# Kernel optimization log

Measured on AMD Instinct MI355X. Metric: run time of the kernel, lower is better.

The kernel has to match this reference:

```python
import jax, jax.numpy as jnp
import numpy as np

OUT_FEATURES = 11008
IN_FEATURES = 4096
GROUP_SIZE = 32
N_GROUPS = OUT_FEATURES * IN_FEATURES // GROUP_SIZE  # 1409024
LEVELS = jnp.array([-1.0, -0.333, 0.333, 1.0], dtype=jnp.float32)


def setup_inputs() -> dict:
    key = jax.random.key(0)
    k1, k2, k3, k4 = jax.random.split(key, 4)
    x = jax.random.normal(k1, (16, IN_FEATURES), dtype=jnp.float32)
    weight_q2 = jax.random.randint(k2, (N_GROUPS, GROUP_SIZE // 4), 0, 256, dtype=jnp.int32)
    weight_norm = jax.random.uniform(k3, (N_GROUPS, 1), dtype=jnp.float32).astype(jnp.float16)
    bias = jax.random.normal(k4, (OUT_FEATURES,), dtype=jnp.float32)
    return {"x": x, "weight_q2": weight_q2, "weight_norm": weight_norm, "bias": bias}


def _dequantize_2bit(packed, norm):
    # packed: [G, group/4] int; element at group-column 4*k+i comes from bits [2i:2i+2) of packed[:, k]
    shifts = jnp.array([0, 2, 4, 6], dtype=jnp.int32)
    codes = (packed[:, :, None] >> shifts[None, None, :]) & 3  # [G, group/4, 4]
    x_q = LEVELS[codes].reshape(packed.shape[0], -1)  # [G, group]
    return x_q * norm.astype(jnp.float32)  # per-group scale


def reference(x, weight_q2, weight_norm, bias):
    weight = _dequantize_2bit(weight_q2, weight_norm).reshape(OUT_FEATURES, IN_FEATURES).astype(x.dtype)
    return x @ weight.T + bias.astype(x.dtype)
```

## Files before the change

### kernel.cpp

```cpp
#include <hip/hip_runtime.h>
#include <hip/hip_fp16.h>

#define OUTF 11008
#define INF  4096
#define NTILES 688

typedef unsigned int uint;
typedef __attribute__((ext_vector_type(8))) _Float16 f16x8;
typedef __attribute__((ext_vector_type(4))) float f32x4;

typedef __attribute__((address_space(1))) void gvoid_t;
typedef __attribute__((address_space(3))) void svoid_t;

union UA { uint4 u4; uint u[4]; f16x8 v; };
union UH { uint u; __half2 h; };
union USH { unsigned short s; __half h; };

#define WAITV(n) asm volatile("s_waitcnt vmcnt(" #n ")" ::: "memory")
#define WAITL()  asm volatile("s_waitcnt lgkmcnt(0)" ::: "memory")
#define SBAR()   __builtin_amdgcn_sched_barrier(0)
#define FENCE()  asm volatile("" ::: "memory")
#define BARRIER() { FENCE(); __builtin_amdgcn_s_barrier(); FENCE(); }

__global__ __launch_bounds__(256, 4) void lin2bit_kernel(
    const float* __restrict__ x, const int* __restrict__ wq,
    const float* __restrict__ wn, const float* __restrict__ bias,
    float* __restrict__ out)
{
  __shared__ __align__(16) char lds[34816];
  char* LUT = lds;
  char* NL  = lds + 2048;
  char* X0  = lds + 10240;
  char* X1  = lds + 18432;
  char* W0  = lds + 26624;
  char* W1  = lds + 30720;

  const int tid = threadIdx.x;
  const int wv  = tid >> 6;
  const int l   = tid & 63;
  const int col = l & 15;
  const int q   = l >> 4;
  const int o0  = (int)blockIdx.x << 4;

  const char* xb  = (const char*)x;
  const char* wqb = (const char*)wq;
  const char* wnb = (const char*)wn;

  {
#pragma unroll
    for (int ii = 0; ii < 2; ++ii) {
      const int i = wv * 2 + ii;
      const int r = 2 * i + (l >> 5);
      const char* src = wnb + (size_t)(o0 + r) * 512 + (((l & 31) ^ (r & 7)) << 4);
      __builtin_amdgcn_global_load_lds((gvoid_t*)src,
                                       (svoid_t*)(NL + i * 1024 + l * 16), 16, 0, 0);
    }
  }
  FENCE();

#define XLOAD(c, xr) { \
    _Pragma("unroll") \
    for (int rr = 0; rr < 4; ++rr) { \
      const int r = wv * 4 + rr; \
      const float* srcp = (const float*)(xb + (size_t)r * 16384 + (size_t)(c) * 1024) + l * 4; \
      asm volatile("global_load_dwordx4 %0, %1, off" \
                   : "=&v"((xr)[rr]) : "v"(srcp) : "memory"); \
    } }

#define XWRITE(buf, xr) { \
    _Pragma("unroll") \
    for (int rr = 0; rr < 4; ++rr) { \
      const int r = wv * 4 + rr; \
      UH h0, h1; \
      h0.h = __floats2half2_rn((xr)[rr].x, (xr)[rr].y); \
      h1.h = __floats2half2_rn((xr)[rr].z, (xr)[rr].w); \
      *(uint2*)((buf) + r * 512 + (((l >> 1) ^ (r & 7)) << 4) + (l & 1) * 8) = \
          make_uint2(h0.u, h1.u); \
    } }

#define WSTAGE(c, buf) { \
    const int r = wv * 4 + (l >> 4); \
    const char* src = wqb + (size_t)(o0 + r) * 4096 + (size_t)(c) * 256 \
                      + (((l & 15) ^ (r & 7)) << 4); \
    __builtin_amdgcn_global_load_lds((gvoid_t*)src, \
                                     (svoid_t*)((buf) + wv * 1024 + l * 16), 16, 0, 0); }

  float4 xrA[4], xrB[4];
  XLOAD(0, xrA);   FENCE();
  WSTAGE(0, W0);   FENCE();
  XLOAD(1, xrB);   FENCE();
  WSTAGE(1, W1);   FENCE();

  {
    USH h0, h1, h2, h3;
    h0.h = __float2half(-1.0f);  h1.h = __float2half(-0.333f);
    h2.h = __float2half(0.333f); h3.h = __float2half(1.0f);
    const uint hv[4] = {h0.s, h1.s, h2.s, h3.s};
#pragma unroll
    for (int e = 0; e < 4; ++e) {
      const int idx = e * 64 + l;
      const uint lo = hv[idx & 3]        | (hv[(idx >> 2) & 3] << 16);
      const uint hi = hv[(idx >> 4) & 3] | (hv[(idx >> 6) & 3] << 16);
      *(uint2*)(LUT + idx * 8) = make_uint2(lo, hi);
    }
  }

  WAITV(5); SBAR();
  XWRITE(X0, xrA);
  WAITL(); BARRIER();

  f32x4 acc = {0.f, 0.f, 0.f, 0.f};
  const int c7 = col & 7;

#define COMPUTE(c, xs, ws) { \
    const float2 nn = *(const float2*)(NL + col * 512 \
                        + ((((c) * 2 + (wv >> 1)) ^ c7) << 4) + (wv & 1) * 8); \
    _Pragma("unroll") \
    for (int jj = 0; jj < 2; ++jj) { \
      const int g = wv * 2 + jj; \
      const float nv = jj ? nn.y : nn.x; \
      UH nvh; nvh.h = __floats2half2_rn(nv, nv); \
      const uint2 p = *(const uint2*)((ws) + col * 256 \
                        + (((g * 2 + (q >> 1)) ^ c7) << 4) + (q & 1) * 8); \
      UA A; A.u4 = *(const uint4*)((xs) + col * 512 + (((g * 4 + q) ^ c7) << 4)); \
      const uint2 e0 = *(const uint2*)(LUT + ((size_t)(uint)p.x << 3)); \
      const uint2 e1 = *(const uint2*)(LUT + ((size_t)(uint)p.y << 3)); \
      UH a0, a1, a2, a3, b0, b1, b2, b3; \
      a0.u = e0.x; a1.u = e0.y; a2.u = e1.x; a3.u = e1.y; \
      b0.h = __hmul2(a0.h, nvh.h); b1.h = __hmul2(a1.h, nvh.h); \
      b2.h = __hmul2(a2.h, nvh.h); b3.h = __hmul2(a3.h, nvh.h); \
      UA B; B.u[0] = b0.u; B.u[1] = b1.u; B.u[2] = b2.u; B.u[3] = b3.u; \
      acc = __builtin_amdgcn_mfma_f32_16x16x32_f16(A.v, B.v, acc, 0, 0, 0); \
    } }

#define ITER_FULL(c, XC, WC, XN, XRC, XRN) \
  COMPUTE(c, XC, WC) \
  XLOAD((c) + 2, XRC);  FENCE(); \
  BARRIER(); \
  WSTAGE((c) + 2, WC);  FENCE(); \
  WAITV(5); SBAR(); \
  XWRITE(XN, XRN); \
  WAITL(); BARRIER();

  ITER_FULL(0,  X0, W0, X1, xrA, xrB)
  ITER_FULL(1,  X1, W1, X0, xrB, xrA)
  ITER_FULL(2,  X0, W0, X1, xrA, xrB)
  ITER_FULL(3,  X1, W1, X0, xrB, xrA)
  ITER_FULL(4,  X0, W0, X1, xrA, xrB)
  ITER_FULL(5,  X1, W1, X0, xrB, xrA)
  ITER_FULL(6,  X0, W0, X1, xrA, xrB)
  ITER_FULL(7,  X1, W1, X0, xrB, xrA)
  ITER_FULL(8,  X0, W0, X1, xrA, xrB)
  ITER_FULL(9,  X1, W1, X0, xrB, xrA)
  ITER_FULL(10, X0, W0, X1, xrA, xrB)
  ITER_FULL(11, X1, W1, X0, xrB, xrA)
  ITER_FULL(12, X0, W0, X1, xrA, xrB)
  ITER_FULL(13, X1, W1, X0, xrB, xrA)
  COMPUTE(14, X0, W0)
  BARRIER();
  WAITV(0); SBAR();
  XWRITE(X1, xrB);
  WAITL(); BARRIER();
  COMPUTE(15, X1, W1)
#undef ITER_FULL
#undef COMPUTE
#undef XLOAD
#undef XWRITE
#undef WSTAGE

  __syncthreads();
  float* red = (float*)lds;
  red[wv * 256 +   0 + l] = acc[0];
  red[wv * 256 +  64 + l] = acc[1];
  red[wv * 256 + 128 + l] = acc[2];
  red[wv * 256 + 192 + l] = acc[3];
  __syncthreads();
  const int t = tid;
  const float s = red[t] + red[256 + t] + red[512 + t] + red[768 + t];
  const int m  = ((t & 63) >> 4) * 4 + (t >> 6);
  const int oc = t & 15;
  out[(size_t)m * OUTF + o0 + oc] = s + bias[o0 + oc];
}

extern "C" void kernel_launch(void* const* d_in, const int* in_sizes, int n_in,
                              void* d_out, int out_size, void* d_ws, size_t ws_size,
                              hipStream_t stream) {
  (void)in_sizes; (void)n_in; (void)out_size; (void)d_ws; (void)ws_size;
  const float* x    = (const float*)d_in[0];
  const int*   wq   = (const int*)d_in[1];
  const float* wn   = (const float*)d_in[2];
  const float* bias = (const float*)d_in[3];
  float*       out  = (float*)d_out;
  lin2bit_kernel<<<dim3(NTILES), dim3(256), 0, stream>>>(x, wq, wn, bias, out);
}
```

Baseline: 19.66 us.

## Process two 16-row output tiles per block to reuse staged activations

Each block now computes 32 output features instead of 16, so the grid is halved and every activation chunk converted to fp16 in LDS feeds two weight tiles and two accumulators. This is meant to cut the redundant per-block x loads and conversions, and the per-block setup. In exchange, LDS grows to about 50KB, the occupancy hint drops from 4 to 3 blocks, and only 344 blocks are launched, which could leave compute units underfilled.

```diff
diff --git a/kernel.cpp b/kernel.cpp
--- a/kernel.cpp
+++ b/kernel.cpp
@@ -3,7 +3,7 @@
 
 #define OUTF 11008
 #define INF  4096
-#define NTILES 688
+#define NBLK 344
 
 typedef unsigned int uint;
 typedef __attribute__((ext_vector_type(8))) _Float16 f16x8;
@@ -22,41 +22,43 @@
 #define FENCE()  asm volatile("" ::: "memory")
 #define BARRIER() { FENCE(); __builtin_amdgcn_s_barrier(); FENCE(); }
 
-__global__ __launch_bounds__(256, 4) void lin2bit_kernel(
+__global__ __launch_bounds__(256, 3) void lin2bit_kernel(
     const float* __restrict__ x, const int* __restrict__ wq,
     const float* __restrict__ wn, const float* __restrict__ bias,
     float* __restrict__ out)
 {
-  __shared__ __align__(16) char lds[34816];
+  __shared__ __align__(16) char lds[51200];
   char* LUT = lds;
-  char* NL  = lds + 2048;
-  char* X0  = lds + 10240;
-  char* X1  = lds + 18432;
-  char* W0  = lds + 26624;
-  char* W1  = lds + 30720;
+  char* NLa = lds + 2048;
+  char* NLb = lds + 10240;
+  char* X0  = lds + 18432;
+  char* X1  = lds + 26624;
+  char* W0a = lds + 34816;
+  char* W0b = lds + 38912;
+  char* W1a = lds + 43008;
+  char* W1b = lds + 47104;
 
   const int tid = threadIdx.x;
   const int wv  = tid >> 6;
   const int l   = tid & 63;
   const int col = l & 15;
   const int q   = l >> 4;
-  const int o0  = (int)blockIdx.x << 4;
+  const int o0a = (int)blockIdx.x << 5;
+  const int o0b = o0a + 16;
 
   const char* xb  = (const char*)x;
   const char* wqb = (const char*)wq;
   const char* wnb = (const char*)wn;
 
-  {
-#pragma unroll
-    for (int ii = 0; ii < 2; ++ii) {
-      const int i = wv * 2 + ii;
-      const int r = 2 * i + (l >> 5);
-      const char* src = wnb + (size_t)(o0 + r) * 512 + (((l & 31) ^ (r & 7)) << 4);
-      __builtin_amdgcn_global_load_lds((gvoid_t*)src,
-                                       (svoid_t*)(NL + i * 1024 + l * 16), 16, 0, 0);
-    }
-  }
-  FENCE();
+#define NSTAGE(o0t, nl) { \
+    _Pragma("unroll") \
+    for (int ii = 0; ii < 2; ++ii) { \
+      const int i = wv * 2 + ii; \
+      const int r = 2 * i + (l >> 5); \
+      const char* src = wnb + (size_t)((o0t) + r) * 512 + (((l & 31) ^ (r & 7)) << 4); \
+      __builtin_amdgcn_global_load_lds((gvoid_t*)src, \
+                                       (svoid_t*)((nl) + i * 1024 + l * 16), 16, 0, 0); \
+    } }
 
 #define XLOAD(c, xr) { \
     _Pragma("unroll") \
@@ -78,18 +80,19 @@
           make_uint2(h0.u, h1.u); \
     } }
 
-#define WSTAGE(c, buf) { \
+#define WSTAGE(c, buf, o0t) { \
     const int r = wv * 4 + (l >> 4); \
-    const char* src = wqb + (size_t)(o0 + r) * 4096 + (size_t)(c) * 256 \
+    const char* src = wqb + (size_t)((o0t) + r) * 4096 + (size_t)(c) * 256 \
                       + (((l & 15) ^ (r & 7)) << 4); \
     __builtin_amdgcn_global_load_lds((gvoid_t*)src, \
                                      (svoid_t*)((buf) + wv * 1024 + l * 16), 16, 0, 0); }
 
   float4 xrA[4], xrB[4];
-  XLOAD(0, xrA);   FENCE();
-  WSTAGE(0, W0);   FENCE();
-  XLOAD(1, xrB);   FENCE();
-  WSTAGE(1, W1);   FENCE();
+  NSTAGE(o0a, NLa);  NSTAGE(o0b, NLb);  FENCE();
+  XLOAD(0, xrA);     FENCE();
+  WSTAGE(0, W0a, o0a); WSTAGE(0, W0b, o0b); FENCE();
+  XLOAD(1, xrB);     FENCE();
+  WSTAGE(1, W1a, o0a); WSTAGE(1, W1b, o0b); FENCE();
 
   {
     USH h0, h1, h2, h3;
@@ -105,15 +108,16 @@
     }
   }
 
-  WAITV(5); SBAR();
+  WAITV(6); SBAR();
   XWRITE(X0, xrA);
   WAITL(); BARRIER();
 
-  f32x4 acc = {0.f, 0.f, 0.f, 0.f};
+  f32x4 accA = {0.f, 0.f, 0.f, 0.f};
+  f32x4 accB = {0.f, 0.f, 0.f, 0.f};
   const int c7 = col & 7;
 
-#define COMPUTE(c, xs, ws) { \
-    const float2 nn = *(const float2*)(NL + col * 512 \
+#define COMPUTE(c, xs, ws, nl, accv) { \
+    const float2 nn = *(const float2*)((nl) + col * 512 \
                         + ((((c) * 2 + (wv >> 1)) ^ c7) << 4) + (wv & 1) * 8); \
     _Pragma("unroll") \
     for (int jj = 0; jj < 2; ++jj) { \
@@ -130,56 +134,75 @@
       b0.h = __hmul2(a0.h, nvh.h); b1.h = __hmul2(a1.h, nvh.h); \
       b2.h = __hmul2(a2.h, nvh.h); b3.h = __hmul2(a3.h, nvh.h); \
       UA B; B.u[0] = b0.u; B.u[1] = b1.u; B.u[2] = b2.u; B.u[3] = b3.u; \
-      acc = __builtin_amdgcn_mfma_f32_16x16x32_f16(A.v, B.v, acc, 0, 0, 0); \
-    } }
-
-#define ITER_FULL(c, XC, WC, XN, XRC, XRN) \
-  COMPUTE(c, XC, WC) \
+      (accv) = __builtin_amdgcn_mfma_f32_16x16x32_f16(A.v, B.v, (accv), 0, 0, 0); \
+    } }
+
+#define ITER_FULL(c, XC, WCa, WCb, XN, XRC, XRN) \
+  COMPUTE(c, XC, WCa, NLa, accA) \
+  COMPUTE(c, XC, WCb, NLb, accB) \
   XLOAD((c) + 2, XRC);  FENCE(); \
   BARRIER(); \
-  WSTAGE((c) + 2, WC);  FENCE(); \
-  WAITV(5); SBAR(); \
+  WSTAGE((c) + 2, WCa, o0a); WSTAGE((c) + 2, WCb, o0b); FENCE(); \
+  WAITV(6); SBAR(); \
   XWRITE(XN, XRN); \
   WAITL(); BARRIER();
 
-  ITER_FULL(0,  X0, W0, X1, xrA, xrB)
-  ITER_FULL(1,  X1, W1, X0, xrB, xrA)
-  ITER_FULL(2,  X0, W0, X1, xrA, xrB)
-  ITER_FULL(3,  X1, W1, X0, xrB, xrA)
-  ITER_FULL(4,  X0, W0, X1, xrA, xrB)
-  ITER_FULL(5,  X1, W1, X0, xrB, xrA)
-  ITER_FULL(6,  X0, W0, X1, xrA, xrB)
-  ITER_FULL(7,  X1, W1, X0, xrB, xrA)
-  ITER_FULL(8,  X0, W0, X1, xrA, xrB)
-  ITER_FULL(9,  X1, W1, X0, xrB, xrA)
-  ITER_FULL(10, X0, W0, X1, xrA, xrB)
-  ITER_FULL(11, X1, W1, X0, xrB, xrA)
-  ITER_FULL(12, X0, W0, X1, xrA, xrB)
-  ITER_FULL(13, X1, W1, X0, xrB, xrA)
-  COMPUTE(14, X0, W0)
+  ITER_FULL(0,  X0, W0a, W0b, X1, xrA, xrB)
+  ITER_FULL(1,  X1, W1a, W1b, X0, xrB, xrA)
+  ITER_FULL(2,  X0, W0a, W0b, X1, xrA, xrB)
+  ITER_FULL(3,  X1, W1a, W1b, X0, xrB, xrA)
+  ITER_FULL(4,  X0, W0a, W0b, X1, xrA, xrB)
+  ITER_FULL(5,  X1, W1a, W1b, X0, xrB, xrA)
+  ITER_FULL(6,  X0, W0a, W0b, X1, xrA, xrB)
+  ITER_FULL(7,  X1, W1a, W1b, X0, xrB, xrA)
+  ITER_FULL(8,  X0, W0a, W0b, X1, xrA, xrB)
+  ITER_FULL(9,  X1, W1a, W1b, X0, xrB, xrA)
+  ITER_FULL(10, X0, W0a, W0b, X1, xrA, xrB)
+  ITER_FULL(11, X1, W1a, W1b, X0, xrB, xrA)
+  ITER_FULL(12, X0, W0a, W0b, X1, xrA, xrB)
+  ITER_FULL(13, X1, W1a, W1b, X0, xrB, xrA)
+  COMPUTE(14, X0, W0a, NLa, accA)
+  COMPUTE(14, X0, W0b, NLb, accB)
   BARRIER();
   WAITV(0); SBAR();
   XWRITE(X1, xrB);
   WAITL(); BARRIER();
-  COMPUTE(15, X1, W1)
+  COMPUTE(15, X1, W1a, NLa, accA)
+  COMPUTE(15, X1, W1b, NLb, accB)
 #undef ITER_FULL
 #undef COMPUTE
 #undef XLOAD
 #undef XWRITE
 #undef WSTAGE
-
-  __syncthreads();
+#undef NSTAGE
+
   float* red = (float*)lds;
-  red[wv * 256 +   0 + l] = acc[0];
-  red[wv * 256 +  64 + l] = acc[1];
-  red[wv * 256 + 128 + l] = acc[2];
-  red[wv * 256 + 192 + l] = acc[3];
-  __syncthreads();
-  const int t = tid;
-  const float s = red[t] + red[256 + t] + red[512 + t] + red[768 + t];
-  const int m  = ((t & 63) >> 4) * 4 + (t >> 6);
-  const int oc = t & 15;
-  out[(size_t)m * OUTF + o0 + oc] = s + bias[o0 + oc];
+  __syncthreads();
+  red[wv * 256 +   0 + l] = accA[0];
+  red[wv * 256 +  64 + l] = accA[1];
+  red[wv * 256 + 128 + l] = accA[2];
+  red[wv * 256 + 192 + l] = accA[3];
+  __syncthreads();
+  {
+    const int t = tid;
+    const float s = red[t] + red[256 + t] + red[512 + t] + red[768 + t];
+    const int m  = ((t & 63) >> 4) * 4 + (t >> 6);
+    const int oc = t & 15;
+    out[(size_t)m * OUTF + o0a + oc] = s + bias[o0a + oc];
+  }
+  __syncthreads();
+  red[wv * 256 +   0 + l] = accB[0];
+  red[wv * 256 +  64 + l] = accB[1];
+  red[wv * 256 + 128 + l] = accB[2];
+  red[wv * 256 + 192 + l] = accB[3];
+  __syncthreads();
+  {
+    const int t = tid;
+    const float s = red[t] + red[256 + t] + red[512 + t] + red[768 + t];
+    const int m  = ((t & 63) >> 4) * 4 + (t >> 6);
+    const int oc = t & 15;
+    out[(size_t)m * OUTF + o0b + oc] = s + bias[o0b + oc];
+  }
 }
 
 extern "C" void kernel_launch(void* const* d_in, const int* in_sizes, int n_in,
@@ -191,5 +214,5 @@
   const float* wn   = (const float*)d_in[2];
   const float* bias = (const float*)d_in[3];
   float*       out  = (float*)d_out;
-  lin2bit_kernel<<<dim3(NTILES), dim3(256), 0, stream>>>(x, wq, wn, bias, out);
+  lin2bit_kernel<<<dim3(NBLK), dim3(256), 0, stream>>>(x, wq, wn, bias, out);
 }
```

Result: slower. 20.23 us (+2.9%).

## Replace LDS dequant LUT with per-group register shift table and preload norms

Applied to the files above, without the earlier changes.

Drops the 256-entry LDS lookup table and its hmul2 scaling. Each group now builds a 64-bit register table of the four pre-scaled fp16 levels and extracts every weight with a 64-bit shift followed by a pack. The per-group norms are loaded straight into registers at kernel start instead of being staged through LDS, which shrinks LDS use and removes two LDS reads per group. The cost is more VALU shift and pack work per element and 32 extra VGPRs to hold the norms. Rounding also changes slightly, since the product is now rounded once from fp32 instead of twice in fp16.

```diff
diff --git a/kernel.cpp b/kernel.cpp
--- a/kernel.cpp
+++ b/kernel.cpp
@@ -6,6 +6,7 @@
 #define NTILES 688
 
 typedef unsigned int uint;
+typedef unsigned long long ull;
 typedef __attribute__((ext_vector_type(8))) _Float16 f16x8;
 typedef __attribute__((ext_vector_type(4))) float f32x4;
 
@@ -14,7 +15,6 @@
 
 union UA { uint4 u4; uint u[4]; f16x8 v; };
 union UH { uint u; __half2 h; };
-union USH { unsigned short s; __half h; };
 
 #define WAITV(n) asm volatile("s_waitcnt vmcnt(" #n ")" ::: "memory")
 #define WAITL()  asm volatile("s_waitcnt lgkmcnt(0)" ::: "memory")
@@ -27,13 +27,11 @@
     const float* __restrict__ wn, const float* __restrict__ bias,
     float* __restrict__ out)
 {
-  __shared__ __align__(16) char lds[34816];
-  char* LUT = lds;
-  char* NL  = lds + 2048;
-  char* X0  = lds + 10240;
-  char* X1  = lds + 18432;
-  char* W0  = lds + 26624;
-  char* W1  = lds + 30720;
+  __shared__ __align__(16) char lds[24576];
+  char* X0 = lds;
+  char* X1 = lds + 8192;
+  char* W0 = lds + 16384;
+  char* W1 = lds + 20480;
 
   const int tid = threadIdx.x;
   const int wv  = tid >> 6;
@@ -44,19 +42,6 @@
 
   const char* xb  = (const char*)x;
   const char* wqb = (const char*)wq;
-  const char* wnb = (const char*)wn;
-
-  {
-#pragma unroll
-    for (int ii = 0; ii < 2; ++ii) {
-      const int i = wv * 2 + ii;
-      const int r = 2 * i + (l >> 5);
-      const char* src = wnb + (size_t)(o0 + r) * 512 + (((l & 31) ^ (r & 7)) << 4);
-      __builtin_amdgcn_global_load_lds((gvoid_t*)src,
-                                       (svoid_t*)(NL + i * 1024 + l * 16), 16, 0, 0);
-    }
-  }
-  FENCE();
 
 #define XLOAD(c, xr) { \
     _Pragma("unroll") \
@@ -85,25 +70,23 @@
     __builtin_amdgcn_global_load_lds((gvoid_t*)src, \
                                      (svoid_t*)((buf) + wv * 1024 + l * 16), 16, 0, 0); }
 
+  float2 nf2[16];
+  {
+    const float* np = wn + (size_t)(o0 + col) * 128 + 2 * wv;
+#pragma unroll
+    for (int c = 0; c < 16; ++c) {
+      const float* p = np + 8 * c;
+      asm volatile("global_load_dwordx2 %0, %1, off"
+                   : "=&v"(nf2[c]) : "v"(p) : "memory");
+    }
+  }
+  FENCE();
+
   float4 xrA[4], xrB[4];
   XLOAD(0, xrA);   FENCE();
   WSTAGE(0, W0);   FENCE();
   XLOAD(1, xrB);   FENCE();
   WSTAGE(1, W1);   FENCE();
-
-  {
-    USH h0, h1, h2, h3;
-    h0.h = __float2half(-1.0f);  h1.h = __float2half(-0.333f);
-    h2.h = __float2half(0.333f); h3.h = __float2half(1.0f);
-    const uint hv[4] = {h0.s, h1.s, h2.s, h3.s};
-#pragma unroll
-    for (int e = 0; e < 4; ++e) {
-      const int idx = e * 64 + l;
-      const uint lo = hv[idx & 3]        | (hv[(idx >> 2) & 3] << 16);
-      const uint hi = hv[(idx >> 4) & 3] | (hv[(idx >> 6) & 3] << 16);
-      *(uint2*)(LUT + idx * 8) = make_uint2(lo, hi);
-    }
-  }
 
   WAITV(5); SBAR();
   XWRITE(X0, xrA);
@@ -113,23 +96,33 @@
   const int c7 = col & 7;
 
 #define COMPUTE(c, xs, ws) { \
-    const float2 nn = *(const float2*)(NL + col * 512 \
-                        + ((((c) * 2 + (wv >> 1)) ^ c7) << 4) + (wv & 1) * 8); \
+    const float2 nn = nf2[c]; \
     _Pragma("unroll") \
     for (int jj = 0; jj < 2; ++jj) { \
       const int g = wv * 2 + jj; \
-      const float nv = jj ? nn.y : nn.x; \
-      UH nvh; nvh.h = __floats2half2_rn(nv, nv); \
+      const float nv  = jj ? nn.y : nn.x; \
+      const float nv3 = nv * 0.333f; \
+      UH tlo, thi; \
+      tlo.h = __floats2half2_rn(-nv, -nv3); \
+      thi.h = __floats2half2_rn(nv3, nv); \
+      const ull T = ((ull)thi.u << 32) | (ull)tlo.u; \
       const uint2 p = *(const uint2*)((ws) + col * 256 \
                         + (((g * 2 + (q >> 1)) ^ c7) << 4) + (q & 1) * 8); \
       UA A; A.u4 = *(const uint4*)((xs) + col * 512 + (((g * 4 + q) ^ c7) << 4)); \
-      const uint2 e0 = *(const uint2*)(LUT + ((size_t)(uint)p.x << 3)); \
-      const uint2 e1 = *(const uint2*)(LUT + ((size_t)(uint)p.y << 3)); \
-      UH a0, a1, a2, a3, b0, b1, b2, b3; \
-      a0.u = e0.x; a1.u = e0.y; a2.u = e1.x; a3.u = e1.y; \
-      b0.h = __hmul2(a0.h, nvh.h); b1.h = __hmul2(a1.h, nvh.h); \
-      b2.h = __hmul2(a2.h, nvh.h); b3.h = __hmul2(a3.h, nvh.h); \
-      UA B; B.u[0] = b0.u; B.u[1] = b1.u; B.u[2] = b2.u; B.u[3] = b3.u; \
+      const uint p0 = p.x << 4, p1 = p.y << 4; \
+      const uint w0 = (uint)(T >> (p0 & 0x30u)); \
+      const uint w1 = (uint)(T >> ((p0 >> 2) & 0x30u)); \
+      const uint w2 = (uint)(T >> ((p0 >> 4) & 0x30u)); \
+      const uint w3 = (uint)(T >> ((p0 >> 6) & 0x30u)); \
+      const uint w4 = (uint)(T >> (p1 & 0x30u)); \
+      const uint w5 = (uint)(T >> ((p1 >> 2) & 0x30u)); \
+      const uint w6 = (uint)(T >> ((p1 >> 4) & 0x30u)); \
+      const uint w7 = (uint)(T >> ((p1 >> 6) & 0x30u)); \
+      UA B; \
+      B.u[0] = (w0 & 0xFFFFu) | (w1 << 16); \
+      B.u[1] = (w2 & 0xFFFFu) | (w3 << 16); \
+      B.u[2] = (w4 & 0xFFFFu) | (w5 << 16); \
+      B.u[3] = (w6 & 0xFFFFu) | (w7 << 16); \
       acc = __builtin_amdgcn_mfma_f32_16x16x32_f16(A.v, B.v, acc, 0, 0, 0); \
     } }
 
```

Result: slower. 25.90 us (+31.7%).
